# Kernel optimization log

Measured on AMD Instinct MI355X. Metric: run time of the kernel, lower is better.

The kernel has to match this reference:

```python
import jax, jax.numpy as jnp
import numpy as np

HIDDEN = 2048
KEY_DIM = 2048
NUM_HEADS = 16
HEAD_DIM = KEY_DIM // NUM_HEADS
ROPE_THETA = 10000.0
EPS = 1e-05


def rms_norm(x, w, eps=EPS):
    var = jnp.mean(x * x, axis=-1, keepdims=True)
    return x * jax.lax.rsqrt(var + eps) * w


def apply_rope(x, theta_base=ROPE_THETA):
    # x: [b, s, h, d]; faithful to the einops repeat '(2 d)' = tile (concat), with
    # even output positions = cos*x1 - sin*x2, odd = sin*x1 + cos*x2.
    b, s, h, d = x.shape
    half = d // 2
    freqs = theta_base ** (jnp.arange(half, dtype=x.dtype) * (-2.0 / d))  # [d/2]
    freqs = jnp.concatenate([freqs, freqs], axis=-1)                      # [d] (tiled)
    pos = jnp.arange(s, dtype=x.dtype)                                    # [s]
    ang = pos[:, None] * freqs[None, :]                                   # [s, d]
    cos = jnp.cos(ang)[None, :, None, :]
    sin = jnp.sin(ang)[None, :, None, :]
    x_even = x[..., 0::2]
    x_odd = x[..., 1::2]
    x1 = jnp.concatenate([x_even, x_even], axis=-1)  # tile '(2 d)'
    x2 = jnp.concatenate([x_odd, x_odd], axis=-1)
    even_mask = (jnp.arange(d) % 2 == 0)[None, None, None, :]
    return jnp.where(even_mask, cos * x1 - sin * x2, sin * x1 + cos * x2)


def setup_inputs() -> dict:
    key = jax.random.key(0)
    ks = jax.random.split(key, 10)
    B, S = 2, 2048
    s_in = 1.0 / np.sqrt(HIDDEN)
    s_k = 1.0 / np.sqrt(KEY_DIM)
    return {
        "x": jax.random.normal(ks[0], (B, S, HIDDEN), dtype=jnp.float32),
        "rms_w": jnp.ones((HIDDEN,), dtype=jnp.float32),
        "wq": jax.random.normal(ks[1], (HIDDEN, KEY_DIM), dtype=jnp.float32) * s_in,
        "bq": jnp.zeros((KEY_DIM,), dtype=jnp.float32),
        "wk": jax.random.normal(ks[2], (HIDDEN, KEY_DIM), dtype=jnp.float32) * s_in,
        "bk": jnp.zeros((KEY_DIM,), dtype=jnp.float32),
        "wv": jax.random.normal(ks[3], (HIDDEN, KEY_DIM), dtype=jnp.float32) * s_in,
        "bv": jnp.zeros((KEY_DIM,), dtype=jnp.float32),
        "wo": jax.random.normal(ks[4], (KEY_DIM, HIDDEN), dtype=jnp.float32) * s_k,
        "bo": jnp.zeros((HIDDEN,), dtype=jnp.float32),
    }


def reference(x, rms_w, wq, bq, wk, bk, wv, bv, wo, bo):
    B, S, _ = x.shape
    residual = x
    xn = rms_norm(x, rms_w)
    q = (xn @ wq + bq).reshape(B, S, NUM_HEADS, HEAD_DIM)
    k = (xn @ wk + bk).reshape(B, S, NUM_HEADS, HEAD_DIM)
    v = (xn @ wv + bv).reshape(B, S, NUM_HEADS, HEAD_DIM)
    q = apply_rope(q)
    k = apply_rope(k)
    scores = jnp.einsum('bshd,bthd->bhst', q, k) / jnp.sqrt(
        jnp.asarray(HEAD_DIM, dtype=x.dtype))
    causal = jnp.tril(jnp.ones((S, S), dtype=bool))[None, None]
    scores = jnp.where(causal, scores, -jnp.inf)
    probs = jax.nn.softmax(scores, axis=-1)
    out = jnp.einsum('bhst,bthd->bshd', probs, v).reshape(B, S, KEY_DIM)
    return out @ wo + bo + residual
```

## Files before the change

### kernel.cpp

```cpp
#include <hip/hip_runtime.h>
#include <stdint.h>
#include <math.h>

#define S_LEN 2048
#define HID 2048
#define NH 16
#define HD 128
#define NROWS 4096
#define SCALE 0.08838834764831845f
#define C2 (0.08838834764831845f * 1.442695040888963f)

typedef unsigned short u16;
typedef __attribute__((ext_vector_type(8))) short short8;
typedef __attribute__((ext_vector_type(4))) float f32x4;
typedef __attribute__((ext_vector_type(16))) float f32x16;
typedef __attribute__((ext_vector_type(4))) unsigned short u16x4;
typedef __attribute__((ext_vector_type(4))) unsigned int u32x4;
typedef __attribute__((ext_vector_type(4))) float float4v;

__device__ __forceinline__ u16 f2bf(float f) {
  union { float f; uint32_t u; } v; v.f = f;
  uint32_t r = v.u + 0x7FFFu + ((v.u >> 16) & 1u);
  return (u16)(r >> 16);
}
__device__ __forceinline__ float bf2f(u16 b) {
  union { uint32_t u; float f; } v; v.u = ((uint32_t)b) << 16;
  return v.f;
}
__device__ __forceinline__ void gl_lds16(const void* g, void* l) {
  __builtin_amdgcn_global_load_lds((const __attribute__((address_space(1))) void*)g,
                                   (__attribute__((address_space(3))) void*)l, 16, 0, 0);
}
__device__ __forceinline__ unsigned cvtpk(float lo, float hi) {
  unsigned r;
  asm("v_cvt_pk_bf16_f32 %0, %1, %2" : "=v"(r) : "v"(lo), "v"(hi));
  return r;
}
__device__ __forceinline__ void plswap(unsigned &a, unsigned &b) {
  asm volatile("v_permlane32_swap_b32 %0, %1" : "+v"(a), "+v"(b));
}

__global__ __launch_bounds__(256) void k_pre(const float* __restrict__ x, const float* __restrict__ rw,
                                             u16* __restrict__ xn,
                                             const float* __restrict__ w0, const float* __restrict__ w1,
                                             const float* __restrict__ w2, const float* __restrict__ w3,
                                             u16* __restrict__ wtbase) {
  int bid = blockIdx.x;
  int tid = threadIdx.x;
  if (bid < 4096) {
    int row = bid;
    const float* xr = x + (size_t)row * HID;
    float4v a = *(const float4v*)(xr + tid * 8);
    float4v b = *(const float4v*)(xr + tid * 8 + 4);
    float s = a[0]*a[0] + a[1]*a[1] + a[2]*a[2] + a[3]*a[3]
            + b[0]*b[0] + b[1]*b[1] + b[2]*b[2] + b[3]*b[3];
    #pragma unroll
    for (int off = 1; off < 64; off <<= 1) s += __shfl_xor(s, off, 64);
    __shared__ float red[4];
    int wv = tid >> 6;
    if ((tid & 63) == 0) red[wv] = s;
    __syncthreads();
    float tot = red[0] + red[1] + red[2] + red[3];
    float r = rsqrtf(tot * (1.0f / HID) + 1e-5f);
    const float* wp = rw + tid * 8;
    u16x4 o0, o1;
    #pragma unroll
    for (int j = 0; j < 4; ++j) { o0[j] = f2bf(a[j] * r * wp[j]); o1[j] = f2bf(b[j] * r * wp[4 + j]); }
    *(u16x4*)(xn + (size_t)row * HID + tid * 8) = o0;
    *(u16x4*)(xn + (size_t)row * HID + tid * 8 + 4) = o1;
  } else {
    int c = bid - 4096;
    int z = c >> 10;
    int rest = c & 1023;
    int n0 = (rest & 31) * 64, k0 = (rest >> 5) * 64;
    const float* w = (z == 0) ? w0 : (z == 1) ? w1 : (z == 2) ? w2 : w3;
    u16* wt = wtbase + (size_t)z * HID * HID;
    __shared__ float t[64][68];
    int cr = tid >> 4;
    int cc = (tid & 15) * 4;
    #pragma unroll
    for (int it = 0; it < 4; ++it) {
      int kk = cr + it * 16;
      float4v v = *(const float4v*)(w + (size_t)(k0 + kk) * HID + n0 + cc);
      t[kk][cc] = v[0]; t[kk][cc + 1] = v[1]; t[kk][cc + 2] = v[2]; t[kk][cc + 3] = v[3];
    }
    __syncthreads();
    #pragma unroll
    for (int it = 0; it < 4; ++it) {
      int nn = cr + it * 16;
      u16x4 o;
      #pragma unroll
      for (int j = 0; j < 4; ++j) o[j] = f2bf(t[cc + j][nn]);
      *(u16x4*)(wt + (size_t)(n0 + nn) * HID + k0 + cc) = o;
    }
  }
}

__global__ __launch_bounds__(256) void k_post(const u16* __restrict__ qh, const u16* __restrict__ kh,
                                              u16* __restrict__ QP, u16* __restrict__ KP,
                                              const u16* __restrict__ vh, u16* __restrict__ VP) {
  int bid = blockIdx.x;
  int tid = threadIdx.x;
  if (bid < 4096) {
    int l = tid & 63, wvv = tid >> 6;
    int rsub = l >> 4, c = l & 15;
    int row = bid * 16 + wvv * 4 + rsub;
    int bh = row >> 11, s = row & 2047;
    int tile = s >> 5, ln = s & 31;
    int ks = c >> 1, hi = c & 1;
    int k3 = ks & 3;
    const u16* qi = qh + (size_t)row * HD + 32 * k3 + 16 * hi;
    const u16* ki = kh + (size_t)row * HD + 32 * k3 + 16 * hi;
    float sn[8], cs[8];
    #pragma unroll
    for (int j = 0; j < 8; ++j) {
      int de = 16 * k3 + 8 * hi + j;
      float freq = exp2f((float)de * -0.20762050593046014f);
      sincosf((float)s * freq, &sn[j], &cs[j]);
    }
    size_t off = ((((size_t)(bh * 64 + tile)) * 8 + ks) * 64 + hi * 32 + ln) * 8;
    {
      short8 a = *(const short8*)(qi);
      short8 b2 = *(const short8*)(qi + 8);
      u16x4 o0, o1;
      #pragma unroll
      for (int j = 0; j < 4; ++j) {
        float x0 = bf2f((u16)a[2 * j]), x1 = bf2f((u16)a[2 * j + 1]);
        o0[j] = f2bf((j & 1) ? (sn[j] * x0 + cs[j] * x1) : (cs[j] * x0 - sn[j] * x1));
      }
      #pragma unroll
      for (int j = 0; j < 4; ++j) {
        int jj = j + 4;
        float x0 = bf2f((u16)b2[2 * j]), x1 = bf2f((u16)b2[2 * j + 1]);
        o1[j] = f2bf((jj & 1) ? (sn[jj] * x0 + cs[jj] * x1) : (cs[jj] * x0 - sn[jj] * x1));
      }
      *(u16x4*)(QP + off) = o0; *(u16x4*)(QP + off + 4) = o1;
    }
    {
      short8 a = *(const short8*)(ki);
      short8 b2 = *(const short8*)(ki + 8);
      u16x4 o0, o1;
      #pragma unroll
      for (int j = 0; j < 4; ++j) {
        float x0 = bf2f((u16)a[2 * j]), x1 = bf2f((u16)a[2 * j + 1]);
        o0[j] = f2bf((j & 1) ? (sn[j] * x0 + cs[j] * x1) : (cs[j] * x0 - sn[j] * x1));
      }
      #pragma unroll
      for (int j = 0; j < 4; ++j) {
        int jj = j + 4;
        float x0 = bf2f((u16)b2[2 * j]), x1 = bf2f((u16)b2[2 * j + 1]);
        o1[j] = f2bf((jj & 1) ? (sn[jj] * x0 + cs[jj] * x1) : (cs[jj] * x0 - sn[jj] * x1));
      }
      *(u16x4*)(KP + off) = o0; *(u16x4*)(KP + off + 4) = o1;
    }
  } else {
    int c = bid - 4096;
    int bx = c & 31;
    int bh = c >> 5;
    __shared__ u16 t[64][136];
    int row = tid >> 2;
    int d0 = (tid & 3) * 32;
    const u16* src = vh + ((size_t)bh * S_LEN + bx * 64 + row) * HD + d0;
    short8 a = *(const short8*)(src);
    short8 b = *(const short8*)(src + 8);
    short8 cc2 = *(const short8*)(src + 16);
    short8 d = *(const short8*)(src + 24);
    *(short8*)(&t[row][d0]) = a;
    *(short8*)(&t[row][d0 + 8]) = b;
    *(short8*)(&t[row][d0 + 16]) = cc2;
    *(short8*)(&t[row][d0 + 24]) = d;
    __syncthreads();
    #pragma unroll
    for (int i = 0; i < 4; ++i) {
      int cid = i * 256 + tid;
      int lp = cid & 63;
      int db = (cid >> 6) & 3;
      int j2 = (cid >> 8) & 1;
      int tl = (cid >> 9) & 1;
      int tg = bx * 2 + tl;
      int tloc = tl * 32 + j2 * 16 + (lp >> 5) * 8;
      int dloc = db * 32 + (lp & 31);
      short8 v;
      #pragma unroll
      for (int jj = 0; jj < 8; ++jj) v[jj] = (short)t[tloc + jj][dloc];
      size_t off = ((((size_t)(bh * 64 + tg) * 2 + j2) * 4 + db) * 64 + lp) * 8;
      *(short8*)(VP + off) = v;
    }
  }
}

__global__ __launch_bounds__(512, 2) void k_gemm_qkv2(const u16* __restrict__ A, const u16* __restrict__ BT,
                                                      const float* __restrict__ bq, const float* __restrict__ bk,
                                                      const float* __restrict__ bv, u16* __restrict__ qkv) {
  extern __shared__ __align__(16) char smraw[];
  u16* sm = (u16*)smraw;
  int bid = blockIdx.x;
  int xcd = bid & 7, loc = bid >> 3;
  int bx = xcd * 3 + loc % 3;
  int by = loc / 3;
  int tid = threadIdx.x;
  int w = tid >> 6, lane = tid & 63;
  int wr = w >> 2, wc = w & 3;
  int lq = lane & 15, lg = lane >> 4;

  f32x4 acc[4][4];
  #pragma unroll
  for (int mi = 0; mi < 4; ++mi)
    #pragma unroll
    for (int ni = 0; ni < 4; ++ni) acc[mi][ni] = (f32x4){0.f, 0.f, 0.f, 0.f};

  const size_t Abase = (size_t)(by * 128) * HID;
  const size_t Bbase = (size_t)(bx * 256) * HID;

  #define STAGE_Q(n)  do { \
    int slot_ = ((n) % 3) * 12288; \
    int kb_ = (n) * 32; \
    { int c_ = tid; int row_ = c_ >> 2; int ch_ = (c_ & 3) ^ ((row_ >> 1) & 3); \
      gl_lds16(A + Abase + (size_t)row_ * HID + kb_ + ch_ * 8, sm + slot_ + c_ * 8); } \
    _Pragma("unroll") \
    for (int it_ = 0; it_ < 2; ++it_) { \
      int c_ = it_ * 512 + tid; int row_ = c_ >> 2; int ch_ = (c_ & 3) ^ ((row_ >> 1) & 3); \
      gl_lds16(BT + Bbase + (size_t)row_ * HID + kb_ + ch_ * 8, sm + slot_ + 4096 + c_ * 8); } \
  } while (0)

  STAGE_Q(0); STAGE_Q(1);
  asm volatile("s_waitcnt vmcnt(3)" ::: "memory");
  __builtin_amdgcn_s_barrier();
  __builtin_amdgcn_sched_barrier(0);

  for (int n = 0; n < 64; ++n) {
    if (n + 2 <= 63) STAGE_Q(n + 2);
    int slot = (n % 3) * 12288;
    const u16* sA = sm + slot;
    const u16* sB = sm + slot + 4096;
    short8 af[4], bf[4];
    #pragma unroll
    for (int mi = 0; mi < 4; ++mi) {
      int ra = wr * 64 + mi * 16 + lq;
      af[mi] = *(const short8*)(sA + ra * 32 + ((lg ^ ((ra >> 1) & 3)) << 3));
    }
    #pragma unroll
    for (int ni = 0; ni < 4; ++ni) {
      int rb = wc * 64 + ni * 16 + lq;
      bf[ni] = *(const short8*)(sB + rb * 32 + ((lg ^ ((rb >> 1) & 3)) << 3));
    }
    __builtin_amdgcn_s_setprio(1);
    #pragma unroll
    for (int mi = 0; mi < 4; ++mi)
      #pragma unroll
      for (int ni = 0; ni < 4; ++ni)
        acc[mi][ni] = __builtin_amdgcn_mfma_f32_16x16x32_bf16(af[mi], bf[ni], acc[mi][ni], 0, 0, 0);
    __builtin_amdgcn_s_setprio(0);
    if (n <= 61) {
      asm volatile("s_waitcnt vmcnt(3)" ::: "memory");
      __builtin_amdgcn_s_barrier();
      __builtin_amdgcn_sched_barrier(0);
    } else if (n == 62) {
      asm volatile("s_waitcnt vmcnt(0)" ::: "memory");
      __builtin_amdgcn_s_barrier();
      __builtin_amdgcn_sched_barrier(0);
    }
  }

  #pragma unroll
  for (int ni = 0; ni < 4; ++ni) {
    int colg = bx * 256 + wc * 64 + ni * 16 + lq;
    int sel = colg >> 11;
    int col = colg & 2047;
    int h = col >> 7, d = col & 127;
    const float* bias = (sel == 0) ? bq : (sel == 1) ? bk : bv;
    float bs = bias[col];
    u16* outp = qkv + (size_t)sel * NROWS * HID;
    #pragma unroll
    for (int mi = 0; mi < 4; ++mi) {
      #pragma unroll
      for (int r = 0; r < 4; ++r) {
        int rowm = by * 128 + wr * 64 + mi * 16 + lg * 4 + r;
        int b = rowm >> 11, s = rowm & 2047;
        outp[(((size_t)(b * NH + h)) * S_LEN + s) * HD + d] = f2bf(acc[mi][ni][r] + bs);
      }
    }
  }
  #undef STAGE_Q
}

__global__ __launch_bounds__(256, 3) void k_gemm_o2(const u16* __restrict__ A, const u16* __restrict__ BT,
                                                    const float* __restrict__ bias,
                                                    const float* __restrict__ resid,
                                                    float* __restrict__ outp) {
  extern __shared__ __align__(16) char smraw[];
  u16* sm = (u16*)smraw;
  int bid = blockIdx.x;
  int xcd = bid & 7, loc = bid >> 3;
  int bx = xcd * 2 + (loc & 1);
  int by = loc >> 1;
  int tid = threadIdx.x;
  int w = tid >> 6, lane = tid & 63;
  int wr = w >> 1, wc = w & 1;
  int lq = lane & 15, lg = lane >> 4;

  f32x4 acc[4][4];
  #pragma unroll
  for (int mi = 0; mi < 4; ++mi)
    #pragma unroll
    for (int ni = 0; ni < 4; ++ni) acc[mi][ni] = (f32x4){0.f, 0.f, 0.f, 0.f};

  const size_t Abase = (size_t)(by * 128) * HID;
  const size_t Bbase = (size_t)(bx * 128) * HID;

  #define STAGE_O(n)  do { \
    int slot_ = ((n) % 3) * 8192; \
    int kb_ = (n) * 32; \
    _Pragma("unroll") \
    for (int it_ = 0; it_ < 2; ++it_) { \
      int c_ = it_ * 256 + tid; int row_ = c_ >> 2; int ch_ = (c_ & 3) ^ ((row_ >> 1) & 3); \
      gl_lds16(A + Abase + (size_t)row_ * HID + kb_ + ch_ * 8, sm + slot_ + c_ * 8); } \
    _Pragma("unroll") \
    for (int it_ = 0; it_ < 2; ++it_) { \
      int c_ = it_ * 256 + tid; int row_ = c_ >> 2; int ch_ = (c_ & 3) ^ ((row_ >> 1) & 3); \
      gl_lds16(BT + Bbase + (size_t)row_ * HID + kb_ + ch_ * 8, sm + slot_ + 4096 + c_ * 8); } \
  } while (0)

  STAGE_O(0); STAGE_O(1);
  asm volatile("s_waitcnt vmcnt(4)" ::: "memory");
  __builtin_amdgcn_s_barrier();
  __builtin_amdgcn_sched_barrier(0);

  for (int n = 0; n < 64; ++n) {
    if (n + 2 <= 63) STAGE_O(n + 2);
    int slot = (n % 3) * 8192;
    const u16* sA = sm + slot;
    const u16* sB = sm + slot + 4096;
    short8 af[4], bf[4];
    #pragma unroll
    for (int mi = 0; mi < 4; ++mi) {
      int ra = wr * 64 + mi * 16 + lq;
      af[mi] = *(const short8*)(sA + ra * 32 + ((lg ^ ((ra >> 1) & 3)) << 3));
    }
    #pragma unroll
    for (int ni = 0; ni < 4; ++ni) {
      int rb = wc * 64 + ni * 16 + lq;
      bf[ni] = *(const short8*)(sB + rb * 32 + ((lg ^ ((rb >> 1) & 3)) << 3));
    }
    __builtin_amdgcn_s_setprio(1);
    #pragma unroll
    for (int mi = 0; mi < 4; ++mi)
      #pragma unroll
      for (int ni = 0; ni < 4; ++ni)
        acc[mi][ni] = __builtin_amdgcn_mfma_f32_16x16x32_bf16(af[mi], bf[ni], acc[mi][ni], 0, 0, 0);
    __builtin_amdgcn_s_setprio(0);
    if (n <= 61) {
      asm volatile("s_waitcnt vmcnt(4)" ::: "memory");
      __builtin_amdgcn_s_barrier();
      __builtin_amdgcn_sched_barrier(0);
    } else if (n == 62) {
      asm volatile("s_waitcnt vmcnt(0)" ::: "memory");
      __builtin_amdgcn_s_barrier();
      __builtin_amdgcn_sched_barrier(0);
    }
  }

  #pragma unroll
  for (int ni = 0; ni < 4; ++ni) {
    int col = bx * 128 + wc * 64 + ni * 16 + lq;
    float bs = bias[col];
    #pragma unroll
    for (int mi = 0; mi < 4; ++mi) {
      #pragma unroll
      for (int r = 0; r < 4; ++r) {
        int rowm = by * 128 + wr * 64 + mi * 16 + lg * 4 + r;
        size_t o = (size_t)rowm * HID + col;
        outp[o] = acc[mi][ni][r] + bs + resid[o];
      }
    }
  }
  #undef STAGE_O
}

__global__ __launch_bounds__(64, 2) void k_attn(const u16* __restrict__ QP, const u16* __restrict__ KP,
                                                const u16* __restrict__ VP, u16* __restrict__ out) {
  int bid = blockIdx.x;
  int rest = bid >> 3;
  int bh = (bid & 7) * 4 + (rest & 3);
  int gg = rest >> 2;
  int qw = (gg < 32) ? (63 - gg) : (gg - 32);
  int b = bh >> 4, h = bh & 15;
  int lane = threadIdx.x;
  int hi = lane >> 5, ln = lane & 31;
  int q0 = qw * 32, qrow = q0 + ln;

  const u16* QPb = QP + ((size_t)(bh * 64 + qw) * 8) * 512 + lane * 8;
  short8 qf[8];
  #pragma unroll
  for (int ks = 0; ks < 8; ++ks) qf[ks] = *(const short8*)(QPb + ks * 512);

  f32x16 oc[4];
  #pragma unroll
  for (int db = 0; db < 4; ++db)
    #pragma unroll
    for (int r = 0; r < 16; ++r) oc[db][r] = 0.f;
  float mr = -3.0e38f, l = 0.f;

  const u16* KPb = KP + ((size_t)bh * 64 * 8) * 512 + lane * 8;
  const u16* VPb = VP + ((size_t)bh * 64 * 8) * 512 + lane * 8;

  int ntile = qw + 1;
  short8 kf[8];
  #pragma unroll
  for (int ks = 0; ks < 8; ++ks) kf[ks] = *(const short8*)(KPb + ks * 512);

  for (int tt = 0; tt < ntile; ++tt) {
    short8 va[8];
    #pragma unroll
    for (int u = 0; u < 8; ++u) va[u] = *(const short8*)(VPb + (size_t)tt * 4096 + u * 512);

    f32x16 st;
    #pragma unroll
    for (int r = 0; r < 16; ++r) st[r] = 0.f;
    __builtin_amdgcn_s_setprio(1);
    #pragma unroll
    for (int ks = 0; ks < 8; ++ks)
      st = __builtin_amdgcn_mfma_f32_32x32x16_bf16(kf[ks], qf[ks], st, 0, 0, 0);
    __builtin_amdgcn_s_setprio(0);

    if (tt + 1 < ntile) {
      #pragma unroll
      for (int ks = 0; ks < 8; ++ks)
        kf[ks] = *(const short8*)(KPb + (size_t)(tt + 1) * 4096 + ks * 512);
    }

    int t0 = tt * 32;
    float sv[16];
    float pm = -3.0e38f;
    bool lastt = (tt == ntile - 1);
    #pragma unroll
    for (int r = 0; r < 16; ++r) {
      float x = st[r];
      if (lastt) {
        int t = t0 + (r & 3) + 8 * (r >> 2) + 4 * hi;
        x = (t <= qrow) ? x : -3.0e38f;
      }
      sv[r] = x;
    }
    #pragma unroll
    for (int r = 0; r < 15; r += 2) pm = fmaxf(fmaxf(pm, sv[r]), sv[r + 1]);
    pm = fmaxf(pm, sv[15]);
    pm = fmaxf(pm, __shfl_xor(pm, 32, 64));
    if (!__all(pm <= mr + 64.0f)) {
      float mnew = fmaxf(mr, pm);
      float al = exp2f((mr - mnew) * C2);
      l *= al;
      #pragma unroll
      for (int db = 0; db < 4; ++db)
        #pragma unroll
        for (int r = 0; r < 16; ++r) oc[db][r] *= al;
      mr = mnew;
    }
    float mc = mr * C2;
    float e[16];
    float rs = 0.f;
    #pragma unroll
    for (int r = 0; r < 16; ++r) {
      e[r] = exp2f(fmaf(sv[r], C2, -mc));
      rs += e[r];
    }
    rs += __shfl_xor(rs, 32, 64);
    l += rs;

    unsigned w0 = cvtpk(e[0], e[1]),   w1 = cvtpk(e[2], e[3]);
    unsigned w2 = cvtpk(e[4], e[5]),   w3 = cvtpk(e[6], e[7]);
    unsigned w4 = cvtpk(e[8], e[9]),   w5 = cvtpk(e[10], e[11]);
    unsigned w6 = cvtpk(e[12], e[13]), w7 = cvtpk(e[14], e[15]);
    plswap(w0, w2); plswap(w1, w3); plswap(w4, w6); plswap(w5, w7);
    u32x4 pw0 = {w0, w1, w2, w3};
    u32x4 pw1 = {w4, w5, w6, w7};
    short8 pb0 = __builtin_bit_cast(short8, pw0);
    short8 pb1 = __builtin_bit_cast(short8, pw1);

    __builtin_amdgcn_s_setprio(1);
    #pragma unroll
    for (int db = 0; db < 4; ++db)
      oc[db] = __builtin_amdgcn_mfma_f32_32x32x16_bf16(va[db], pb0, oc[db], 0, 0, 0);
    #pragma unroll
    for (int db = 0; db < 4; ++db)
      oc[db] = __builtin_amdgcn_mfma_f32_32x32x16_bf16(va[4 + db], pb1, oc[db], 0, 0, 0);
    __builtin_amdgcn_s_setprio(0);
  }

  float inv = 1.0f / l;
  size_t ob = ((size_t)(b * S_LEN + qrow)) * HID + h * HD;
  #pragma unroll
  for (int db = 0; db < 4; ++db) {
    #pragma unroll
    for (int g = 0; g < 4; ++g) {
      u16x4 pk;
      #pragma unroll
      for (int j = 0; j < 4; ++j) pk[j] = f2bf(oc[db][4 * g + j] * inv);
      *(u16x4*)(out + ob + db * 32 + 8 * g + 4 * hi) = pk;
    }
  }
}

extern "C" void kernel_launch(void* const* d_in, const int* in_sizes, int n_in,
                              void* d_out, int out_size, void* d_ws, size_t ws_size,
                              hipStream_t stream) {
  const float* x    = (const float*)d_in[0];
  const float* rmsw = (const float*)d_in[1];
  const float* wq   = (const float*)d_in[2];
  const float* bq   = (const float*)d_in[3];
  const float* wk   = (const float*)d_in[4];
  const float* bk   = (const float*)d_in[5];
  const float* wv   = (const float*)d_in[6];
  const float* bv   = (const float*)d_in[7];
  const float* wo   = (const float*)d_in[8];
  const float* bo   = (const float*)d_in[9];

  char* ws = (char*)d_ws;
  const size_t SZ = (size_t)NROWS * HID * 2;
  const size_t WSZ = (size_t)HID * HID * 2;
  u16* xn   = (u16*)(ws);
  u16* wqkT = (u16*)(ws + SZ);
  u16* woT  = (u16*)(ws + SZ + 3 * WSZ);
  u16* qhm  = (u16*)(ws + SZ + 4 * WSZ);
  u16* khm  = (u16*)(ws + SZ + 4 * WSZ + SZ);
  u16* vhm  = (u16*)(ws + SZ + 4 * WSZ + 2 * SZ);
  u16* QP   = xn;
  u16* KP   = wqkT;
  u16* VP   = khm;
  u16* ao   = qhm;

  k_pre<<<dim3(8192), dim3(256), 0, stream>>>(x, rmsw, xn, wq, wk, wv, wo, wqkT);
  k_gemm_qkv2<<<dim3(768), dim3(512), 73728, stream>>>(xn, wqkT, bq, bk, bv, qhm);
  k_post<<<dim3(5120), dim3(256), 0, stream>>>(qhm, khm, QP, KP, vhm, VP);
  k_attn<<<dim3(2048), dim3(64), 0, stream>>>(QP, KP, VP, ao);
  k_gemm_o2<<<dim3(512), dim3(256), 49152, stream>>>(ao, woT, bo, x, (float*)d_out);
}
```

Baseline: 263.4 us.

## Split GEMM mainloop into two halves interleaving A/B prefetch with MFMA

Both the QKV and output-projection GEMM main loops now issue the A-tile prefetch, compute the first half of the N fragments, hit an extra barrier, then issue the B-tile prefetch and compute the second half. The goal is to spread global-to-LDS issue across the MFMA stream and lower the register pressure from holding all B fragments at once. In exchange each k-step gets an extra workgroup barrier, and the waitcnt counts are left unchanged even though the load issue order is now different.

```diff
diff --git a/kernel.cpp b/kernel.cpp
--- a/kernel.cpp
+++ b/kernel.cpp
@@ -212,44 +212,64 @@
   const size_t Abase = (size_t)(by * 128) * HID;
   const size_t Bbase = (size_t)(bx * 256) * HID;
 
-  #define STAGE_Q(n)  do { \
+  #define STAGE_QA(n)  do { \
     int slot_ = ((n) % 3) * 12288; \
     int kb_ = (n) * 32; \
-    { int c_ = tid; int row_ = c_ >> 2; int ch_ = (c_ & 3) ^ ((row_ >> 1) & 3); \
-      gl_lds16(A + Abase + (size_t)row_ * HID + kb_ + ch_ * 8, sm + slot_ + c_ * 8); } \
+    int c_ = tid; int row_ = c_ >> 2; int ch_ = (c_ & 3) ^ ((row_ >> 1) & 3); \
+    gl_lds16(A + Abase + (size_t)row_ * HID + kb_ + ch_ * 8, sm + slot_ + c_ * 8); \
+  } while (0)
+  #define STAGE_QB(n)  do { \
+    int slot_ = ((n) % 3) * 12288; \
+    int kb_ = (n) * 32; \
     _Pragma("unroll") \
     for (int it_ = 0; it_ < 2; ++it_) { \
       int c_ = it_ * 512 + tid; int row_ = c_ >> 2; int ch_ = (c_ & 3) ^ ((row_ >> 1) & 3); \
       gl_lds16(BT + Bbase + (size_t)row_ * HID + kb_ + ch_ * 8, sm + slot_ + 4096 + c_ * 8); } \
   } while (0)
 
-  STAGE_Q(0); STAGE_Q(1);
+  STAGE_QA(0); STAGE_QB(0); STAGE_QA(1); STAGE_QB(1);
   asm volatile("s_waitcnt vmcnt(3)" ::: "memory");
   __builtin_amdgcn_s_barrier();
   __builtin_amdgcn_sched_barrier(0);
 
   for (int n = 0; n < 64; ++n) {
-    if (n + 2 <= 63) STAGE_Q(n + 2);
     int slot = (n % 3) * 12288;
     const u16* sA = sm + slot;
     const u16* sB = sm + slot + 4096;
-    short8 af[4], bf[4];
+    if (n + 2 <= 63) STAGE_QA(n + 2);
+    short8 af[4], bf01[2];
     #pragma unroll
     for (int mi = 0; mi < 4; ++mi) {
       int ra = wr * 64 + mi * 16 + lq;
       af[mi] = *(const short8*)(sA + ra * 32 + ((lg ^ ((ra >> 1) & 3)) << 3));
     }
     #pragma unroll
-    for (int ni = 0; ni < 4; ++ni) {
+    for (int ni = 0; ni < 2; ++ni) {
       int rb = wc * 64 + ni * 16 + lq;
-      bf[ni] = *(const short8*)(sB + rb * 32 + ((lg ^ ((rb >> 1) & 3)) << 3));
+      bf01[ni] = *(const short8*)(sB + rb * 32 + ((lg ^ ((rb >> 1) & 3)) << 3));
     }
     __builtin_amdgcn_s_setprio(1);
     #pragma unroll
     for (int mi = 0; mi < 4; ++mi)
       #pragma unroll
-      for (int ni = 0; ni < 4; ++ni)
-        acc[mi][ni] = __builtin_amdgcn_mfma_f32_16x16x32_bf16(af[mi], bf[ni], acc[mi][ni], 0, 0, 0);
+      for (int ni = 0; ni < 2; ++ni)
+        acc[mi][ni] = __builtin_amdgcn_mfma_f32_16x16x32_bf16(af[mi], bf01[ni], acc[mi][ni], 0, 0, 0);
+    __builtin_amdgcn_s_setprio(0);
+    __builtin_amdgcn_s_barrier();
+    __builtin_amdgcn_sched_barrier(0);
+    if (n + 2 <= 63) STAGE_QB(n + 2);
+    short8 bf23[2];
+    #pragma unroll
+    for (int ni = 0; ni < 2; ++ni) {
+      int rb = wc * 64 + (ni + 2) * 16 + lq;
+      bf23[ni] = *(const short8*)(sB + rb * 32 + ((lg ^ ((rb >> 1) & 3)) << 3));
+    }
+    __builtin_amdgcn_s_setprio(1);
+    #pragma unroll
+    for (int mi = 0; mi < 4; ++mi)
+      #pragma unroll
+      for (int ni = 0; ni < 2; ++ni)
+        acc[mi][ni + 2] = __builtin_amdgcn_mfma_f32_16x16x32_bf16(af[mi], bf23[ni], acc[mi][ni + 2], 0, 0, 0);
     __builtin_amdgcn_s_setprio(0);
     if (n <= 61) {
       asm volatile("s_waitcnt vmcnt(3)" ::: "memory");
@@ -281,7 +301,8 @@
       }
     }
   }
-  #undef STAGE_Q
+  #undef STAGE_QA
+  #undef STAGE_QB
 }
 
 __global__ __launch_bounds__(256, 3) void k_gemm_o2(const u16* __restrict__ A, const u16* __restrict__ BT,
@@ -308,46 +329,66 @@
   const size_t Abase = (size_t)(by * 128) * HID;
   const size_t Bbase = (size_t)(bx * 128) * HID;
 
-  #define STAGE_O(n)  do { \
+  #define STAGE_OA(n)  do { \
     int slot_ = ((n) % 3) * 8192; \
     int kb_ = (n) * 32; \
     _Pragma("unroll") \
     for (int it_ = 0; it_ < 2; ++it_) { \
       int c_ = it_ * 256 + tid; int row_ = c_ >> 2; int ch_ = (c_ & 3) ^ ((row_ >> 1) & 3); \
       gl_lds16(A + Abase + (size_t)row_ * HID + kb_ + ch_ * 8, sm + slot_ + c_ * 8); } \
+  } while (0)
+  #define STAGE_OB(n)  do { \
+    int slot_ = ((n) % 3) * 8192; \
+    int kb_ = (n) * 32; \
     _Pragma("unroll") \
     for (int it_ = 0; it_ < 2; ++it_) { \
       int c_ = it_ * 256 + tid; int row_ = c_ >> 2; int ch_ = (c_ & 3) ^ ((row_ >> 1) & 3); \
       gl_lds16(BT + Bbase + (size_t)row_ * HID + kb_ + ch_ * 8, sm + slot_ + 4096 + c_ * 8); } \
   } while (0)
 
-  STAGE_O(0); STAGE_O(1);
+  STAGE_OA(0); STAGE_OB(0); STAGE_OA(1); STAGE_OB(1);
   asm volatile("s_waitcnt vmcnt(4)" ::: "memory");
   __builtin_amdgcn_s_barrier();
   __builtin_amdgcn_sched_barrier(0);
 
   for (int n = 0; n < 64; ++n) {
-    if (n + 2 <= 63) STAGE_O(n + 2);
     int slot = (n % 3) * 8192;
     const u16* sA = sm + slot;
     const u16* sB = sm + slot + 4096;
-    short8 af[4], bf[4];
+    if (n + 2 <= 63) STAGE_OA(n + 2);
+    short8 af[4], bf01[2];
     #pragma unroll
     for (int mi = 0; mi < 4; ++mi) {
       int ra = wr * 64 + mi * 16 + lq;
       af[mi] = *(const short8*)(sA + ra * 32 + ((lg ^ ((ra >> 1) & 3)) << 3));
     }
     #pragma unroll
-    for (int ni = 0; ni < 4; ++ni) {
+    for (int ni = 0; ni < 2; ++ni) {
       int rb = wc * 64 + ni * 16 + lq;
-      bf[ni] = *(const short8*)(sB + rb * 32 + ((lg ^ ((rb >> 1) & 3)) << 3));
+      bf01[ni] = *(const short8*)(sB + rb * 32 + ((lg ^ ((rb >> 1) & 3)) << 3));
     }
     __builtin_amdgcn_s_setprio(1);
     #pragma unroll
     for (int mi = 0; mi < 4; ++mi)
       #pragma unroll
-      for (int ni = 0; ni < 4; ++ni)
-        acc[mi][ni] = __builtin_amdgcn_mfma_f32_16x16x32_bf16(af[mi], bf[ni], acc[mi][ni], 0, 0, 0);
+      for (int ni = 0; ni < 2; ++ni)
+        acc[mi][ni] = __builtin_amdgcn_mfma_f32_16x16x32_bf16(af[mi], bf01[ni], acc[mi][ni], 0, 0, 0);
+    __builtin_amdgcn_s_setprio(0);
+    __builtin_amdgcn_s_barrier();
+    __builtin_amdgcn_sched_barrier(0);
+    if (n + 2 <= 63) STAGE_OB(n + 2);
+    short8 bf23[2];
+    #pragma unroll
+    for (int ni = 0; ni < 2; ++ni) {
+      int rb = wc * 64 + (ni + 2) * 16 + lq;
+      bf23[ni] = *(const short8*)(sB + rb * 32 + ((lg ^ ((rb >> 1) & 3)) << 3));
+    }
+    __builtin_amdgcn_s_setprio(1);
+    #pragma unroll
+    for (int mi = 0; mi < 4; ++mi)
+      #pragma unroll
+      for (int ni = 0; ni < 2; ++ni)
+        acc[mi][ni + 2] = __builtin_amdgcn_mfma_f32_16x16x32_bf16(af[mi], bf23[ni], acc[mi][ni + 2], 0, 0, 0);
     __builtin_amdgcn_s_setprio(0);
     if (n <= 61) {
       asm volatile("s_waitcnt vmcnt(4)" ::: "memory");
@@ -374,7 +415,8 @@
       }
     }
   }
-  #undef STAGE_O
+  #undef STAGE_OA
+  #undef STAGE_OB
 }
 
 __global__ __launch_bounds__(64, 2) void k_attn(const u16* __restrict__ QP, const u16* __restrict__ KP,
```

After: 266.2 us. About the same (+1.0%).

## Double QKV GEMM k-tile to 64 and split B loads across two compute halves

Applied to the files above, without the earlier changes.

The QKV projection GEMM now loads 64-wide k-tiles, with a 3-slot ring of 147 KB LDS and an 8-chunk XOR swizzle. Each iteration splits into two halves, each computing half of the N fragments, and the B-tile loads for the stage two ahead are interleaved between the halves. The aim is to halve the number of barrier/wait iterations and overlap global-to-LDS traffic with MFMA work more finely. In exchange, occupancy drops to one 512-thread block per CU, so there is less latency hiding across blocks.

```diff
diff --git a/kernel.cpp b/kernel.cpp
--- a/kernel.cpp
+++ b/kernel.cpp
@@ -189,7 +189,7 @@
   }
 }
 
-__global__ __launch_bounds__(512, 2) void k_gemm_qkv2(const u16* __restrict__ A, const u16* __restrict__ BT,
+__global__ __launch_bounds__(512, 1) void k_gemm_qkv2(const u16* __restrict__ A, const u16* __restrict__ BT,
                                                       const float* __restrict__ bq, const float* __restrict__ bk,
                                                       const float* __restrict__ bv, u16* __restrict__ qkv) {
   extern __shared__ __align__(16) char smraw[];
@@ -212,54 +212,83 @@
   const size_t Abase = (size_t)(by * 128) * HID;
   const size_t Bbase = (size_t)(bx * 256) * HID;
 
-  #define STAGE_Q(n)  do { \
-    int slot_ = ((n) % 3) * 12288; \
-    int kb_ = (n) * 32; \
-    { int c_ = tid; int row_ = c_ >> 2; int ch_ = (c_ & 3) ^ ((row_ >> 1) & 3); \
-      gl_lds16(A + Abase + (size_t)row_ * HID + kb_ + ch_ * 8, sm + slot_ + c_ * 8); } \
+  #define STAGE_A(n)  do { \
+    int slot_ = ((n) % 3) * 24576; \
+    int kb_ = (n) * 64; \
     _Pragma("unroll") \
     for (int it_ = 0; it_ < 2; ++it_) { \
-      int c_ = it_ * 512 + tid; int row_ = c_ >> 2; int ch_ = (c_ & 3) ^ ((row_ >> 1) & 3); \
-      gl_lds16(BT + Bbase + (size_t)row_ * HID + kb_ + ch_ * 8, sm + slot_ + 4096 + c_ * 8); } \
+      int c_ = it_ * 512 + tid; int row_ = c_ >> 3; int cs_ = (c_ & 7) ^ (row_ & 7); \
+      gl_lds16(A + Abase + (size_t)row_ * HID + kb_ + cs_ * 8, sm + slot_ + c_ * 8); } \
   } while (0)
-
-  STAGE_Q(0); STAGE_Q(1);
-  asm volatile("s_waitcnt vmcnt(3)" ::: "memory");
+  #define STAGE_B(n, h)  do { \
+    int slot_ = ((n) % 3) * 24576; \
+    int kb_ = (n) * 64; \
+    _Pragma("unroll") \
+    for (int it_ = 0; it_ < 2; ++it_) { \
+      int c_ = it_ * 512 + tid; int row_ = c_ >> 3; int cs_ = (c_ & 7) ^ (row_ & 7); \
+      gl_lds16(BT + Bbase + (size_t)(128 * (h) + row_) * HID + kb_ + cs_ * 8, \
+               sm + slot_ + 8192 + 8192 * (h) + c_ * 8); } \
+  } while (0)
+
+  STAGE_A(0); STAGE_B(0, 0); STAGE_B(0, 1);
+  STAGE_A(1); STAGE_B(1, 0); STAGE_B(1, 1);
+  asm volatile("s_waitcnt vmcnt(6)" ::: "memory");
   __builtin_amdgcn_s_barrier();
   __builtin_amdgcn_sched_barrier(0);
 
-  for (int n = 0; n < 64; ++n) {
-    if (n + 2 <= 63) STAGE_Q(n + 2);
-    int slot = (n % 3) * 12288;
+  for (int t = 0; t < 32; ++t) {
+    int slot = (t % 3) * 24576;
     const u16* sA = sm + slot;
-    const u16* sB = sm + slot + 4096;
-    short8 af[4], bf[4];
+    const u16* sB = sm + slot + 8192;
+    if (t == 31) asm volatile("s_waitcnt vmcnt(0)" ::: "memory");
+    else         asm volatile("s_waitcnt vmcnt(6)" ::: "memory");
+    short8 af[4][2], bf0[2][2];
     #pragma unroll
     for (int mi = 0; mi < 4; ++mi) {
       int ra = wr * 64 + mi * 16 + lq;
-      af[mi] = *(const short8*)(sA + ra * 32 + ((lg ^ ((ra >> 1) & 3)) << 3));
-    }
-    #pragma unroll
-    for (int ni = 0; ni < 4; ++ni) {
-      int rb = wc * 64 + ni * 16 + lq;
-      bf[ni] = *(const short8*)(sB + rb * 32 + ((lg ^ ((rb >> 1) & 3)) << 3));
-    }
+      #pragma unroll
+      for (int ks = 0; ks < 2; ++ks)
+        af[mi][ks] = *(const short8*)(sA + ra * 64 + (((ks * 4 + lg) ^ (ra & 7)) << 3));
+    }
+    #pragma unroll
+    for (int nl = 0; nl < 2; ++nl) {
+      int rb = wc * 64 + nl * 16 + lq;
+      #pragma unroll
+      for (int ks = 0; ks < 2; ++ks)
+        bf0[nl][ks] = *(const short8*)(sB + rb * 64 + (((ks * 4 + lg) ^ (rb & 7)) << 3));
+    }
+    if (t + 2 < 32) { STAGE_A(t + 2); STAGE_B(t + 2, 0); }
     __builtin_amdgcn_s_setprio(1);
     #pragma unroll
-    for (int mi = 0; mi < 4; ++mi)
-      #pragma unroll
-      for (int ni = 0; ni < 4; ++ni)
-        acc[mi][ni] = __builtin_amdgcn_mfma_f32_16x16x32_bf16(af[mi], bf[ni], acc[mi][ni], 0, 0, 0);
+    for (int ks = 0; ks < 2; ++ks)
+      #pragma unroll
+      for (int mi = 0; mi < 4; ++mi)
+        #pragma unroll
+        for (int nl = 0; nl < 2; ++nl)
+          acc[mi][nl] = __builtin_amdgcn_mfma_f32_16x16x32_bf16(af[mi][ks], bf0[nl][ks], acc[mi][nl], 0, 0, 0);
     __builtin_amdgcn_s_setprio(0);
-    if (n <= 61) {
-      asm volatile("s_waitcnt vmcnt(3)" ::: "memory");
-      __builtin_amdgcn_s_barrier();
-      __builtin_amdgcn_sched_barrier(0);
-    } else if (n == 62) {
-      asm volatile("s_waitcnt vmcnt(0)" ::: "memory");
-      __builtin_amdgcn_s_barrier();
-      __builtin_amdgcn_sched_barrier(0);
-    }
+    __builtin_amdgcn_s_barrier();
+    __builtin_amdgcn_sched_barrier(0);
+    short8 bf1[2][2];
+    #pragma unroll
+    for (int nl = 0; nl < 2; ++nl) {
+      int rb = wc * 64 + (nl + 2) * 16 + lq;
+      #pragma unroll
+      for (int ks = 0; ks < 2; ++ks)
+        bf1[nl][ks] = *(const short8*)(sB + rb * 64 + (((ks * 4 + lg) ^ (rb & 7)) << 3));
+    }
+    if (t + 2 < 32) STAGE_B(t + 2, 1);
+    __builtin_amdgcn_s_setprio(1);
+    #pragma unroll
+    for (int ks = 0; ks < 2; ++ks)
+      #pragma unroll
+      for (int mi = 0; mi < 4; ++mi)
+        #pragma unroll
+        for (int nl = 0; nl < 2; ++nl)
+          acc[mi][nl + 2] = __builtin_amdgcn_mfma_f32_16x16x32_bf16(af[mi][ks], bf1[nl][ks], acc[mi][nl + 2], 0, 0, 0);
+    __builtin_amdgcn_s_setprio(0);
+    __builtin_amdgcn_s_barrier();
+    __builtin_amdgcn_sched_barrier(0);
   }
 
   #pragma unroll
@@ -281,7 +310,8 @@
       }
     }
   }
-  #undef STAGE_Q
+  #undef STAGE_A
+  #undef STAGE_B
 }
 
 __global__ __launch_bounds__(256, 3) void k_gemm_o2(const u16* __restrict__ A, const u16* __restrict__ BT,
@@ -530,7 +560,7 @@
   u16* ao   = qhm;
 
   k_pre<<<dim3(8192), dim3(256), 0, stream>>>(x, rmsw, xn, wq, wk, wv, wo, wqkT);
-  k_gemm_qkv2<<<dim3(768), dim3(512), 73728, stream>>>(xn, wqkT, bq, bk, bv, qhm);
+  k_gemm_qkv2<<<dim3(768), dim3(512), 147456, stream>>>(xn, wqkT, bq, bk, bv, qhm);
   k_post<<<dim3(5120), dim3(256), 0, stream>>>(qhm, khm, QP, KP, vhm, VP);
   k_attn<<<dim3(2048), dim3(64), 0, stream>>>(QP, KP, VP, ao);
   k_gemm_o2<<<dim3(512), dim3(256), 49152, stream>>>(ao, woT, bo, x, (float*)d_out);
```

New measurement: 255.2 us. 1.03x faster.
